# Kernel tuning notes

Hardware: AMD Instinct MI355X
Metric: run time of the kernel (lower is better)

The kernel has to match this reference:

```python
import jax, jax.numpy as jnp
import numpy as np

B, IN_UNITS, C, U, K = 32, 16, 8192, 32, 16
NUM_ITERS = 3


def setup_inputs() -> dict:
    key = jax.random.key(0)
    k1, k2 = jax.random.split(key)
    x = jax.random.normal(k1, (B, IN_UNITS, C), dtype=jnp.float32)
    # W corresponds to the torch parameter of shape (1, C, U, K, IN_UNITS), leading 1 dropped
    W = jax.random.normal(k2, (C, U, K, IN_UNITS), dtype=jnp.float32)
    return {"x": x, "W": W}


def reference(x, W):
    batch = x.shape[0]
    # u_hat[b,c,u,k] = sum_i W[c,u,k,i] * x[b,i,c]   (torch: W @ x after transpose/stack)
    u_hat = jnp.einsum('cuki,bic->bcuk', W, x)
    b_ij = jnp.zeros((C, U), dtype=x.dtype)
    v = None
    for _ in range(NUM_ITERS):
        c_ij = jax.nn.softmax(b_ij, axis=0)            # softmax over in_channels (dim=1 in torch)
        s = jnp.einsum('cu,bcuk->buk', c_ij, u_hat)    # weighted sum over channels
        # squash: note the original sums over dim=2 of (B,1,U,K,1) == the num_units axis
        mag_sq = jnp.sum(s ** 2, axis=1, keepdims=True)  # (B,1,K)
        mag = jnp.sqrt(mag_sq)
        v = mag_sq / (1.0 + mag_sq) * (s / mag)          # (B,U,K)
        # agreement: mean over batch of <u_hat, v>
        a = jnp.einsum('bcuk,buk->cu', u_hat, v) / batch
        b_ij = b_ij + a
    return v[..., None]  # matches torch output (B, num_units, unit_size, 1)
```

## Files before the change

kernel.cpp:

```cpp
#include <hip/hip_runtime.h>

#define CC   8192
#define UU   32
#define KK   16
#define BB   32
#define INU  16
#define UK   512
#define CPB  32
#define NBLK 512

typedef __attribute__((ext_vector_type(4))) float  f32x4;
typedef __attribute__((ext_vector_type(4))) __bf16 bf16x4;
typedef __attribute__((ext_vector_type(8))) __bf16 bf16x8;

__global__ __launch_bounds__(256) void transpose_x(
    const float* __restrict__ x, float* __restrict__ xT)
{
    __shared__ float tile[64][65];
    const int bc = blockIdx.x & 127;
    const int bb = blockIdx.x >> 7;
    const int c0 = bc * 64, bi0 = bb * 64;
    const int tx = threadIdx.x & 63, ty = threadIdx.x >> 6;
#pragma unroll
    for (int j = 0; j < 64; j += 4)
        tile[ty + j][tx] = x[(size_t)(bi0 + ty + j) * CC + (c0 + tx)];
    __syncthreads();
#pragma unroll
    for (int j = 0; j < 64; j += 4)
        xT[(size_t)(c0 + ty + j) * (BB * INU) + (bi0 + tx)] = tile[tx][ty + j];
}

__device__ inline bf16x4 hi4(f32x4 f)
{
    bf16x4 h;
    h[0] = (__bf16)f[0]; h[1] = (__bf16)f[1];
    h[2] = (__bf16)f[2]; h[3] = (__bf16)f[3];
    return h;
}
__device__ inline bf16x4 lo4(f32x4 f, bf16x4 h)
{
    bf16x4 l;
    l[0] = (__bf16)(f[0] - (float)h[0]); l[1] = (__bf16)(f[1] - (float)h[1]);
    l[2] = (__bf16)(f[2] - (float)h[2]); l[3] = (__bf16)(f[3] - (float)h[3]);
    return l;
}
#define CAT8(a, b) __builtin_shufflevector((a), (b), 0, 1, 2, 3, 4, 5, 6, 7)

__global__ __launch_bounds__(512, 4) void fused_mfma(
    const float* __restrict__ W, const float* __restrict__ xT,
    const float* __restrict__ v_in, float* __restrict__ b_io,
    float* __restrict__ S, float* __restrict__ Z)
{
    const int tid  = threadIdx.x;
    const int w    = tid >> 6;
    const int lane = tid & 63;
    const int col  = lane & 15;
    const int g    = lane >> 4;
    const int c0   = (blockIdx.x >> 1) * CPB;
    const int u0   = (blockIdx.x & 1) * 16 + w * 2;
    const int loff = col * 16 + g * 4;

    const float* vbase = v_in + (size_t)col * UK + u0 * KK + g * 4;
    f32x4 vfA0 = *(const f32x4*)(vbase);
    f32x4 vfB0 = *(const f32x4*)(vbase + KK);
    f32x4 vfA1 = *(const f32x4*)(vbase + 16 * UK);
    f32x4 vfB1 = *(const f32x4*)(vbase + 16 * UK + KK);

    f32x4 sA0 = {0.f, 0.f, 0.f, 0.f}, sA1 = sA0, sB0 = sA0, sB1 = sA0;
    float zl0 = 0.f, zl1 = 0.f;

    f32x4 wf0, wf1, xf0, xf1;
    {
        const float* wb = W + ((size_t)c0 * UU + u0) * (KK * INU) + loff;
        wf0 = *(const f32x4*)(wb);
        wf1 = *(const f32x4*)(wb + 256);
        const float* xb = xT + (size_t)c0 * (BB * INU) + loff;
        xf0 = *(const f32x4*)(xb);
        xf1 = *(const f32x4*)(xb + 256);
    }

    const bf16x4 zb4 = {(__bf16)0.f, (__bf16)0.f, (__bf16)0.f, (__bf16)0.f};
    const f32x4  fz4 = {0.f, 0.f, 0.f, 0.f};

    for (int cc = 0; cc < CPB; ++cc) {
        const int c = c0 + cc;
        const bool have_next = (cc + 1 < CPB);

        float2 bv = *(const float2*)(b_io + (size_t)c * UU + u0);

        f32x4 wn0, wn1, xn0, xn1;
        if (have_next) {
            const float* wb = W + ((size_t)(c + 1) * UU + u0) * (KK * INU) + loff;
            wn0 = *(const f32x4*)(wb);
            wn1 = *(const f32x4*)(wb + 256);
            const float* xb = xT + (size_t)(c + 1) * (BB * INU) + loff;
            xn0 = *(const f32x4*)(xb);
            xn1 = *(const f32x4*)(xb + 256);
        }

        bf16x4 xh0 = hi4(xf0), xl0 = lo4(xf0, xh0);
        bf16x4 xh1 = hi4(xf1), xl1 = lo4(xf1, xh1);
        bf16x8 B1a = CAT8(xh0, xh0);
        bf16x8 B2a = CAT8(xl0, zb4);
        bf16x8 B1b = CAT8(xh1, xh1);
        bf16x8 B2b = CAT8(xl1, zb4);

        bf16x4 wh0 = hi4(wf0), wl0 = lo4(wf0, wh0);
        bf16x4 wh1 = hi4(wf1), wl1 = lo4(wf1, wh1);
        bf16x8 Aa = CAT8(wh0, wl0);
        bf16x8 Ab = CAT8(wh1, wl1);

        f32x4 aA0 = __builtin_amdgcn_mfma_f32_16x16x32_bf16(Aa, B1a, fz4, 0, 0, 0);
        aA0       = __builtin_amdgcn_mfma_f32_16x16x32_bf16(Aa, B2a, aA0, 0, 0, 0);
        f32x4 aA1 = __builtin_amdgcn_mfma_f32_16x16x32_bf16(Aa, B1b, fz4, 0, 0, 0);
        aA1       = __builtin_amdgcn_mfma_f32_16x16x32_bf16(Aa, B2b, aA1, 0, 0, 0);
        f32x4 aB0 = __builtin_amdgcn_mfma_f32_16x16x32_bf16(Ab, B1a, fz4, 0, 0, 0);
        aB0       = __builtin_amdgcn_mfma_f32_16x16x32_bf16(Ab, B2a, aB0, 0, 0, 0);
        f32x4 aB1 = __builtin_amdgcn_mfma_f32_16x16x32_bf16(Ab, B1b, fz4, 0, 0, 0);
        aB1       = __builtin_amdgcn_mfma_f32_16x16x32_bf16(Ab, B2b, aB1, 0, 0, 0);

        f32x4 d0 = aA0 * vfA0 + aA1 * vfA1;
        f32x4 d1 = aB0 * vfB0 + aB1 * vfB1;
        float p0 = (d0[0] + d0[1]) + (d0[2] + d0[3]);
        float p1 = (d1[0] + d1[1]) + (d1[2] + d1[3]);
#pragma unroll
        for (int off = 1; off < 64; off <<= 1) {
            p0 += __shfl_xor(p0, off);
            p1 += __shfl_xor(p1, off);
        }

        const float bn0 = bv.x + p0 * (1.0f / (float)BB);
        const float bn1 = bv.y + p1 * (1.0f / (float)BB);
        const float e0 = __expf(bn0);
        const float e1 = __expf(bn1);
        zl0 += e0; zl1 += e1;
        if (lane == 0) *(float2*)(b_io + (size_t)c * UU + u0) = make_float2(bn0, bn1);

        sA0 += aA0 * e0;  sA1 += aA1 * e0;
        sB0 += aB0 * e1;  sB1 += aB1 * e1;

        if (have_next) { wf0 = wn0; wf1 = wn1; xf0 = xn0; xf1 = xn1; }
    }

    {
        float* sb0 = S + (size_t)col * UK + u0 * KK + g * 4;
        float* sb1 = sb0 + 16 * UK;
        atomicAdd(sb0 + 0,      sA0[0]); atomicAdd(sb0 + 1,      sA0[1]);
        atomicAdd(sb0 + 2,      sA0[2]); atomicAdd(sb0 + 3,      sA0[3]);
        atomicAdd(sb0 + KK + 0, sB0[0]); atomicAdd(sb0 + KK + 1, sB0[1]);
        atomicAdd(sb0 + KK + 2, sB0[2]); atomicAdd(sb0 + KK + 3, sB0[3]);
        atomicAdd(sb1 + 0,      sA1[0]); atomicAdd(sb1 + 1,      sA1[1]);
        atomicAdd(sb1 + 2,      sA1[2]); atomicAdd(sb1 + 3,      sA1[3]);
        atomicAdd(sb1 + KK + 0, sB1[0]); atomicAdd(sb1 + KK + 1, sB1[1]);
        atomicAdd(sb1 + KK + 2, sB1[2]); atomicAdd(sb1 + KK + 3, sB1[3]);
    }
    if (lane == 0) {
        atomicAdd(Z + u0,     zl0);
        atomicAdd(Z + u0 + 1, zl1);
    }
}

__global__ __launch_bounds__(512, 2) void fused_pass_lds(
    const float* __restrict__ x, const float* __restrict__ W,
    const float* __restrict__ v_in, float* __restrict__ b_io,
    float* __restrict__ S, float* __restrict__ Z)
{
    __shared__ float xs[16 * 516];

    const int t   = threadIdx.x;
    const int bid = blockIdx.x;
    const int c0  = bid * 32;
    const int u   = t >> 4;
    const int k   = t & 15;

    float v[BB], Sl[BB], uh[BB];
#pragma unroll
    for (int b = 0; b < BB; ++b) { v[b] = v_in[b * UK + t]; Sl[b] = 0.f; }
    float zloc = 0.f;

    float4 w0, w1, w2, w3;
    {
        const float4* p = (const float4*)(W + ((size_t)c0 * UK + t) * INU);
        w0 = p[0]; w1 = p[1]; w2 = p[2]; w3 = p[3];
    }

    for (int cc = 0; cc < 32; ++cc) {
        if ((cc & 15) == 0) {
            __syncthreads();
            const int cbase = c0 + (cc & ~15);
            for (int j = 0; j < 16; ++j) {
                int idx = j * 512 + t;
                int ccl = idx & 15;
                int bi  = idx >> 4;
                xs[ccl * 516 + bi] = x[bi * CC + cbase + ccl];
            }
            __syncthreads();
        }

        float4 n0, n1, n2, n3;
        const bool have_next = (cc + 1 < 32);
        if (have_next) {
            const float4* p = (const float4*)(W + ((size_t)(c0 + cc + 1) * UK + t) * INU);
            n0 = p[0]; n1 = p[1]; n2 = p[2]; n3 = p[3];
        }

        const float* xrow = &xs[(cc & 15) * 516];
        float ap = 0.f;
#pragma unroll
        for (int b = 0; b < BB; ++b) {
            const float4* xr = (const float4*)(xrow + b * INU);
            float4 x0 = xr[0], x1 = xr[1], x2 = xr[2], x3 = xr[3];
            float h;
            h = w0.x * x0.x;
            h = fmaf(w0.y, x0.y, h); h = fmaf(w0.z, x0.z, h); h = fmaf(w0.w, x0.w, h);
            h = fmaf(w1.x, x1.x, h); h = fmaf(w1.y, x1.y, h);
            h = fmaf(w1.z, x1.z, h); h = fmaf(w1.w, x1.w, h);
            h = fmaf(w2.x, x2.x, h); h = fmaf(w2.y, x2.y, h);
            h = fmaf(w2.z, x2.z, h); h = fmaf(w2.w, x2.w, h);
            h = fmaf(w3.x, x3.x, h); h = fmaf(w3.y, x3.y, h);
            h = fmaf(w3.z, x3.z, h); h = fmaf(w3.w, x3.w, h);
            uh[b] = h;
            ap = fmaf(h, v[b], ap);
        }

        ap += __shfl_xor(ap, 8);
        ap += __shfl_xor(ap, 4);
        ap += __shfl_xor(ap, 2);
        ap += __shfl_xor(ap, 1);

        const int c = c0 + cc;
        float bnew = b_io[c * UU + u] + ap * (1.0f / (float)BB);
        float e = __expf(bnew);
        zloc += e;
        if (k == 0) b_io[c * UU + u] = bnew;

#pragma unroll
        for (int b = 0; b < BB; ++b) Sl[b] = fmaf(e, uh[b], Sl[b]);

        if (have_next) { w0 = n0; w1 = n1; w2 = n2; w3 = n3; }
    }

#pragma unroll
    for (int b = 0; b < BB; ++b) atomicAdd(S + b * UK + t, Sl[b]);
    if (k == 0) atomicAdd(Z + u, zloc);
}

__global__ void squash_k(const float* __restrict__ S, const float* __restrict__ Z,
                         float* __restrict__ vout)
{
    __shared__ float z_sh[UU];
    __shared__ float s2_sh[UK];
    __shared__ float mag_sh[KK];

    const int b = blockIdx.x;
    const int t = threadIdx.x;

    if (t < UU) z_sh[t] = Z[t];
    float ssum = S[b * UK + t];
    __syncthreads();

    float s = ssum / z_sh[t >> 4];
    s2_sh[t] = s * s;
    __syncthreads();

    if (t < KK) {
        float m = 0.f;
        for (int uu = 0; uu < UU; ++uu) m += s2_sh[uu * KK + t];
        mag_sh[t] = m;
    }
    __syncthreads();

    float msq = mag_sh[t & 15];
    float out = (msq / (1.0f + msq)) * s / sqrtf(msq);
    vout[b * UK + t] = out;
}

extern "C" void kernel_launch(void* const* d_in, const int* in_sizes, int n_in,
                              void* d_out, int out_size, void* d_ws, size_t ws_size,
                              hipStream_t stream)
{
    const float* x = (const float*)d_in[0];
    const float* W = (const float*)d_in[1];
    float* out = (float*)d_out;

    char* ws = (char*)d_ws;

    const size_t XT_OFF = 0x140400;
    const size_t NEED   = XT_OFF + (size_t)CC * BB * INU * 4;

    if (ws_size >= NEED) {
        float* S3  = (float*)(ws);
        float* Z3  = (float*)(ws + 0x30000);
        float* vb  = (float*)(ws + 0x30200);
        float* bio = (float*)(ws + 0x40200);
        float* xT  = (float*)(ws + XT_OFF);

        hipMemsetAsync(ws, 0, 0x140200, stream);
        transpose_x<<<1024, 256, 0, stream>>>(x, xT);

        for (int pass = 0; pass < 3; ++pass) {
            float* S = S3 + (size_t)pass * (BB * UK);
            float* Z = Z3 + (size_t)pass * 32;
            fused_mfma<<<NBLK, 512, 0, stream>>>(W, xT, vb, bio, S, Z);
            float* vo = (pass == 2) ? out : vb;
            squash_k<<<BB, UK, 0, stream>>>(S, Z, vo);
        }
    } else {
        float* S   = (float*)(ws);
        float* Z   = (float*)(ws + 65536);
        float* vb  = (float*)(ws + 65536 + 256);
        float* bio = (float*)(ws + 65536 + 256 + 65536);

        hipMemsetAsync(vb,  0, BB * UK * 4, stream);
        hipMemsetAsync(bio, 0, CC * UU * 4, stream);

        for (int pass = 0; pass < 3; ++pass) {
            hipMemsetAsync(S, 0, BB * UK * 4, stream);
            hipMemsetAsync(Z, 0, UU * 4, stream);
            fused_pass_lds<<<256, 512, 0, stream>>>(x, W, vb, bio, S, Z);
            float* vo = (pass == 2) ? out : vb;
            squash_k<<<BB, UK, 0, stream>>>(S, Z, vo);
        }
    }
}
```

Baseline: 779.3 us.

## Stream W tiles through per-wave LDS ring via async global_load_lds

```diff
diff --git a/kernel.cpp b/kernel.cpp
--- a/kernel.cpp
+++ b/kernel.cpp
@@ -9,9 +9,16 @@
 #define CPB  32
 #define NBLK 512
 
+#define RING_SLOTS 4
+#define STAGE_DIST 3
+#define SLICE      2048
+
 typedef __attribute__((ext_vector_type(4))) float  f32x4;
 typedef __attribute__((ext_vector_type(4))) __bf16 bf16x4;
 typedef __attribute__((ext_vector_type(8))) __bf16 bf16x8;
+
+typedef __attribute__((address_space(1))) const void gas_t;
+typedef __attribute__((address_space(3))) void las_t;
 
 __global__ __launch_bounds__(256) void transpose_x(
     const float* __restrict__ x, float* __restrict__ xT)
@@ -51,6 +58,8 @@
     const float* __restrict__ v_in, float* __restrict__ b_io,
     float* __restrict__ S, float* __restrict__ Z)
 {
+    __shared__ char ring[8 * RING_SLOTS * SLICE];
+
     const int tid  = threadIdx.x;
     const int w    = tid >> 6;
     const int lane = tid & 63;
@@ -60,6 +69,8 @@
     const int u0   = (blockIdx.x & 1) * 16 + w * 2;
     const int loff = col * 16 + g * 4;
 
+    char* wring = ring + w * (RING_SLOTS * SLICE);
+
     const float* vbase = v_in + (size_t)col * UK + u0 * KK + g * 4;
     f32x4 vfA0 = *(const f32x4*)(vbase);
     f32x4 vfB0 = *(const f32x4*)(vbase + KK);
@@ -69,15 +80,25 @@
     f32x4 sA0 = {0.f, 0.f, 0.f, 0.f}, sA1 = sA0, sB0 = sA0, sB1 = sA0;
     float zl0 = 0.f, zl1 = 0.f;
 
-    f32x4 wf0, wf1, xf0, xf1;
+#define STAGE(CCI)                                                            \
+    {                                                                         \
+        const int   _slot = (CCI) & (RING_SLOTS - 1);                         \
+        const float* _gp  = W + ((size_t)(c0 + (CCI)) * UU + u0) * 256;       \
+        __builtin_amdgcn_global_load_lds(                                     \
+            (gas_t*)(_gp + lane * 4),                                         \
+            (las_t*)(wring + _slot * SLICE), 16, 0, 0);                       \
+        __builtin_amdgcn_global_load_lds(                                     \
+            (gas_t*)(_gp + 256 + lane * 4),                                   \
+            (las_t*)(wring + _slot * SLICE + 1024), 16, 0, 0);                \
+    }
+
+    f32x4 xf0, xf1, xn0, xn1;
     {
-        const float* wb = W + ((size_t)c0 * UU + u0) * (KK * INU) + loff;
-        wf0 = *(const f32x4*)(wb);
-        wf1 = *(const f32x4*)(wb + 256);
         const float* xb = xT + (size_t)c0 * (BB * INU) + loff;
         xf0 = *(const f32x4*)(xb);
         xf1 = *(const f32x4*)(xb + 256);
     }
+    STAGE(0) STAGE(1) STAGE(2)
 
     const bf16x4 zb4 = {(__bf16)0.f, (__bf16)0.f, (__bf16)0.f, (__bf16)0.f};
     const f32x4  fz4 = {0.f, 0.f, 0.f, 0.f};
@@ -87,16 +108,22 @@
         const bool have_next = (cc + 1 < CPB);
 
         float2 bv = *(const float2*)(b_io + (size_t)c * UU + u0);
-
-        f32x4 wn0, wn1, xn0, xn1;
         if (have_next) {
-            const float* wb = W + ((size_t)(c + 1) * UU + u0) * (KK * INU) + loff;
-            wn0 = *(const f32x4*)(wb);
-            wn1 = *(const f32x4*)(wb + 256);
             const float* xb = xT + (size_t)(c + 1) * (BB * INU) + loff;
             xn0 = *(const f32x4*)(xb);
             xn1 = *(const f32x4*)(xb + 256);
         }
+
+        if (cc + STAGE_DIST < CPB) {
+            STAGE(cc + STAGE_DIST)
+            asm volatile("s_waitcnt vmcnt(6)" ::: "memory");
+        } else {
+            asm volatile("s_waitcnt vmcnt(0)" ::: "memory");
+        }
+
+        const char* slab = wring + (cc & (RING_SLOTS - 1)) * SLICE;
+        f32x4 wf0 = *(const f32x4*)(slab + col * 64 + g * 16);
+        f32x4 wf1 = *(const f32x4*)(slab + 1024 + col * 64 + g * 16);
 
         bf16x4 xh0 = hi4(xf0), xl0 = lo4(xf0, xh0);
         bf16x4 xh1 = hi4(xf1), xl1 = lo4(xf1, xh1);
@@ -139,7 +166,7 @@
         sA0 += aA0 * e0;  sA1 += aA1 * e0;
         sB0 += aB0 * e1;  sB1 += aB1 * e1;
 
-        if (have_next) { wf0 = wn0; wf1 = wn1; xf0 = xn0; xf1 = xn1; }
+        if (have_next) { xf0 = xn0; xf1 = xn1; }
     }
 
     {
```

Result: no change. 786.0 us (+0.9%).
